# Optimization experiments

Hardware: AMD Instinct MI355X
Metric: run time of the kernel (lower is better)

## Reference

```python
import jax, jax.numpy as jnp
import numpy as np

B, S, E, H, D = 4, 2048, 1024, 16, 64   # batch, seq, embed, heads, head_dim
NUM_BUCKETS, MAX_DISTANCE = 32, 128


def _relative_position_bucket(relative_position, num_buckets, max_distance):
    # causal T5-style bucketing
    max_exact = num_buckets // 2
    max_distance = max(max_distance, max_exact + 1)
    distance = jnp.maximum(-relative_position, 0)
    is_small = distance < max_exact
    safe_distance = jnp.maximum(distance, 1)
    log_scale = jnp.log(safe_distance / max_exact) / jnp.log(max_distance / max_exact)
    large_bucket = max_exact + (log_scale * (num_buckets - max_exact)).astype(jnp.int32)
    large_bucket = jnp.minimum(large_bucket, num_buckets - 1)
    return jnp.where(is_small, distance, large_bucket)


def setup_inputs() -> dict:
    key = jax.random.key(0)
    ks = jax.random.split(key, 7)
    w_scale = 1.0 / np.sqrt(E)
    inputs_q = jax.random.normal(ks[0], (B, S, E), jnp.float32)
    inputs_kv = jax.random.normal(ks[1], (B, S, E), jnp.float32)
    Wq = jax.random.normal(ks[2], (E, H * D), jnp.float32) * w_scale
    Wk = jax.random.normal(ks[3], (E, H * D), jnp.float32) * w_scale
    Wv = jax.random.normal(ks[4], (E, H * D), jnp.float32) * w_scale
    Wo = jax.random.normal(ks[5], (H * D, E), jnp.float32) * (1.0 / np.sqrt(H * D))
    rel_bias = jax.random.normal(ks[6], (H, NUM_BUCKETS), jnp.float32) * 0.02
    mask = jnp.tril(jnp.ones((S, S), dtype=bool))[None, None]  # [1,1,Q,K] causal
    return {"inputs_q": inputs_q, "inputs_kv": inputs_kv, "mask": mask,
            "Wq": Wq, "Wk": Wk, "Wv": Wv, "Wo": Wo, "rel_bias": rel_bias}


def reference(inputs_q, inputs_kv, mask, Wq, Wk, Wv, Wo, rel_bias):
    batch, q_len, embed = inputs_q.shape
    k_len = inputs_kv.shape[1]
    q = (inputs_q @ Wq).reshape(batch, q_len, H, D)
    k = (inputs_kv @ Wk).reshape(batch, k_len, H, D)
    v = (inputs_kv @ Wv).reshape(batch, k_len, H, D)
    attention = jnp.einsum("bqhd,bkhd->bhqk", q, k) * (1.0 / jnp.sqrt(D))
    # T5 relative position bias
    rel_pos = jnp.arange(k_len, dtype=jnp.int32)[None, :] - jnp.arange(q_len, dtype=jnp.int32)[:, None]
    bucket = _relative_position_bucket(rel_pos, NUM_BUCKETS, MAX_DISTANCE)  # [Q,K]
    attention = attention + jnp.take(rel_bias, bucket, axis=1)[None]  # [1,H,Q,K]
    attention = jnp.where(mask, attention, jnp.finfo(jnp.float32).min)
    normalized = jax.nn.softmax(attention, axis=-1)
    output = jnp.einsum("bhqk,bkhd->bqhd", normalized, v).reshape(batch, q_len, H * D)
    return output @ Wo
```

## Files before the change

### kernel.cpp

```cpp
#include <hip/hip_runtime.h>

typedef unsigned short u16;
typedef unsigned int u32;
typedef __bf16 bf16x8 __attribute__((ext_vector_type(8)));
typedef float f32x2 __attribute__((ext_vector_type(2)));
typedef float f32x4 __attribute__((ext_vector_type(4)));
typedef float f32x16 __attribute__((ext_vector_type(16)));

#define S_LEN 2048
#define EMB 1024
#define NH 16
#define HD 64
#define LOG2E 1.44269504088896f
#define QSCALE (0.125f * LOG2E)
#define THRL 11.5415603f
#define FB(r) ((((r) ^ ((r) >> 2))) & 3)

__device__ __forceinline__ u16 f2bf(float f) {
  union { float f; unsigned u; } v; v.f = f;
  unsigned r = (v.u + 0x7fffu + ((v.u >> 16) & 1u)) >> 16;
  return (u16)r;
}

__device__ __forceinline__ u32 packbf(float a, float b) {
  union { __bf16 h[2]; u32 u; } x;
  x.h[0] = (__bf16)a; x.h[1] = (__bf16)b;
  return x.u;
}

__device__ __forceinline__ void g2l16(const void* g, void* l) {
  __builtin_amdgcn_global_load_lds(
      (const unsigned int __attribute__((address_space(1)))*)g,
      (unsigned int __attribute__((address_space(3)))*)l, 16, 0, 0);
}

__device__ __forceinline__ float permswap_max(float a) {
  auto r = __builtin_amdgcn_permlane32_swap(__float_as_int(a), __float_as_int(a), false, false);
  return fmaxf(__int_as_float(r[0]), __int_as_float(r[1]));
}
__device__ __forceinline__ float permswap_add(float a) {
  auto r = __builtin_amdgcn_permlane32_swap(__float_as_int(a), __float_as_int(a), false, false);
  return __int_as_float(r[0]) + __int_as_float(r[1]);
}

__device__ __forceinline__ void phase_end() {
  asm volatile("s_waitcnt lgkmcnt(0)" ::: "memory");
  asm volatile("s_waitcnt vmcnt(0)" ::: "memory");
  __builtin_amdgcn_s_barrier();
  asm volatile("" ::: "memory");
}


__global__ void cvt_bf16_2(const float* __restrict__ aq, const float* __restrict__ akv,
                           u16* __restrict__ dq, u16* __restrict__ dkv) {
  int i = blockIdx.x * blockDim.x + threadIdx.x;
  const float4* s;
  ushort4* d;
  int j;
  if (i < 2097152) {
    s = (const float4*)aq; d = (ushort4*)dq; j = i;
  } else {
    s = (const float4*)akv; d = (ushort4*)dkv; j = i - 2097152;
  }
  float4 f = s[j];
  ushort4 o;
  o.x = f2bf(f.x); o.y = f2bf(f.y); o.z = f2bf(f.z); o.w = f2bf(f.w);
  d[j] = o;
}

__global__ void transcvt4(const float* __restrict__ W0, const float* __restrict__ W1,
                          const float* __restrict__ W2, const float* __restrict__ W3,
                          u16* __restrict__ Dqkv, u16* __restrict__ Do) {
  __shared__ float t[32][33];
  const int z = blockIdx.z;
  const float* W = (z == 0) ? W0 : (z == 1) ? W1 : (z == 2) ? W2 : W3;
  u16* Wt = (z < 3) ? (Dqkv + (size_t)z * 1048576) : Do;
  int k0 = blockIdx.x * 32, n0 = blockIdx.y * 32;
  int tx = threadIdx.x & 31, ty = threadIdx.x >> 5;
#pragma unroll
  for (int i = 0; i < 4; i++) t[ty + i * 8][tx] = W[(k0 + ty + i * 8) * 1024 + n0 + tx];
  __syncthreads();
#pragma unroll
  for (int i = 0; i < 4; i++) Wt[(n0 + ty + i * 8) * 1024 + k0 + tx] = f2bf(t[tx][ty + i * 8]);
}

__global__ void build_bias(const float* __restrict__ rel, float* __restrict__ tbl) {
  int i = blockIdx.x * 256 + threadIdx.x;
  int h = i >> 11, dist = i & 2047;
  int bk;
  if (dist < 16) {
    bk = dist;
  } else {
    float ls = logf((float)dist * (1.0f / 16.0f)) * (1.0f / logf(8.0f));
    bk = 16 + (int)(ls * 16.0f);
    if (bk > 31) bk = 31;
  }
  tbl[i] = rel[h * 32 + bk] * LOG2E;
}


__global__ __launch_bounds__(256, 4) void gemm_qkv(const u16* __restrict__ Aq,
                                                   const u16* __restrict__ Akv,
                                                   const u16* __restrict__ Wt,
                                                   u16* __restrict__ QKV, float qscale) {
  constexpr int K = EMB;
  __shared__ u16 As[2][128 * 32];
  __shared__ u16 Bs[2][128 * 32];

  const int bid = blockIdx.x;
  const int xcd = bid & 7, idx = bid >> 3;
  const int mt = xcd * 8 + (idx & 7);
  const int nt = idx >> 3;
  const int m0 = mt * 128;
  const int n0 = nt * 128;
  const int mat = n0 >> 10;
  const u16* A = (mat == 0) ? Aq : Akv;

  const int tid = threadIdx.x;
  const int lane = tid & 63;
  const int wid = tid >> 6;
  const int wm = (wid >> 1) * 64;
  const int wn = (wid & 1) * 64;
  const int la = lane & 15;
  const int lg = lane >> 4;

  const int r0 = tid >> 2;
  const int c0 = ((tid & 3) ^ FB(r0)) * 8;
  const u16* gA = A + (size_t)(m0 + r0) * K + c0;
  const u16* gB = Wt + (size_t)(n0 + r0) * K + c0;

  f32x4 acc[4][4] = {};

  g2l16(gA, As[0] + tid * 8);
  g2l16(gA + 64 * K, As[0] + tid * 8 + 2048);
  g2l16(gB, Bs[0] + tid * 8);
  g2l16(gB + 64 * K, Bs[0] + tid * 8 + 2048);
  gA += 32;
  gB += 32;
  asm volatile("s_waitcnt vmcnt(0)" ::: "memory");
  __builtin_amdgcn_s_barrier();
  asm volatile("" ::: "memory");

  for (int t = 0; t < 32; ++t) {
    const int cur = t & 1;
    if (t < 31) {
      u16* lA = As[cur ^ 1] + tid * 8;
      u16* lB = Bs[cur ^ 1] + tid * 8;
      g2l16(gA, lA);
      g2l16(gA + 64 * K, lA + 2048);
      g2l16(gB, lB);
      g2l16(gB + 64 * K, lB + 2048);
      gA += 32;
      gB += 32;
    }

    bf16x8 af[4], bb[4];
#pragma unroll
    for (int mf = 0; mf < 4; mf++) {
      int row = wm + mf * 16 + la;
      af[mf] = *(const bf16x8*)&As[cur][row * 32 + ((lg ^ FB(row)) << 3)];
    }
#pragma unroll
    for (int nf = 0; nf < 4; nf++) {
      int row = wn + nf * 16 + la;
      bb[nf] = *(const bf16x8*)&Bs[cur][row * 32 + ((lg ^ FB(row)) << 3)];
    }
    __builtin_amdgcn_s_setprio(1);
#pragma unroll
    for (int mf = 0; mf < 4; mf++)
#pragma unroll
      for (int nf = 0; nf < 4; nf++)
        acc[mf][nf] =
            __builtin_amdgcn_mfma_f32_16x16x32_bf16(af[mf], bb[nf], acc[mf][nf], 0, 0, 0);
    __builtin_amdgcn_s_setprio(0);

    phase_end();
  }

  const float sc = (mat == 0) ? qscale : 1.0f;
#pragma unroll
  for (int mf = 0; mf < 4; mf++)
#pragma unroll
    for (int nf = 0; nf < 4; nf++)
#pragma unroll
      for (int r = 0; r < 4; r++) {
        int m = m0 + wm + mf * 16 + lg * 4 + r;
        int n = n0 + wn + nf * 16 + la;
        float v = acc[mf][nf][r] * sc;
        int b = m >> 11, s = m & 2047, h = (n >> 6) & 15, d = n & 63;
        size_t base = (size_t)mat << 23;
        if (mat < 2)
          QKV[base + (((size_t)(b * 16 + h) * 2048 + s) << 6) + d] = f2bf(v);
        else
          QKV[base + (((size_t)(b * 16 + h) * 64 + d) << 11) + s] = f2bf(v);
      }
}


__global__ __launch_bounds__(256, 4) void gemm_out(const u16* __restrict__ A,
                                                   const u16* __restrict__ Bt,
                                                   float* __restrict__ C) {
  constexpr int K = EMB;
  __shared__ u16 As[2][128 * 32];
  __shared__ u16 Bs[2][128 * 32];
  const int bid = blockIdx.x;
  const int xcd = bid & 7, idx = bid >> 3;
  const int mt = xcd * 8 + (idx & 7);
  const int nt = idx >> 3;
  const int m0 = mt * 128;
  const int n0 = nt * 128;
  const int tid = threadIdx.x;
  const int lane = tid & 63;
  const int wid = tid >> 6;
  const int wm = (wid >> 1) * 64;
  const int wn = (wid & 1) * 64;
  const int la = lane & 15;
  const int lg = lane >> 4;

  const int r0 = tid >> 2;
  const int c0 = ((tid & 3) ^ FB(r0)) * 8;
  const u16* gA = A + (size_t)(m0 + r0) * K + c0;
  const u16* gB = Bt + (size_t)(n0 + r0) * K + c0;

  f32x4 acc[4][4] = {};

  g2l16(gA, As[0] + tid * 8);
  g2l16(gA + 64 * K, As[0] + tid * 8 + 2048);
  g2l16(gB, Bs[0] + tid * 8);
  g2l16(gB + 64 * K, Bs[0] + tid * 8 + 2048);
  gA += 32;
  gB += 32;
  asm volatile("s_waitcnt vmcnt(0)" ::: "memory");
  __builtin_amdgcn_s_barrier();
  asm volatile("" ::: "memory");

  for (int t = 0; t < 32; ++t) {
    const int cur = t & 1;
    if (t < 31) {
      u16* lA = As[cur ^ 1] + tid * 8;
      u16* lB = Bs[cur ^ 1] + tid * 8;
      g2l16(gA, lA);
      g2l16(gA + 64 * K, lA + 2048);
      g2l16(gB, lB);
      g2l16(gB + 64 * K, lB + 2048);
      gA += 32;
      gB += 32;
    }

    bf16x8 af[4], bb[4];
#pragma unroll
    for (int mf = 0; mf < 4; mf++) {
      int row = wm + mf * 16 + la;
      af[mf] = *(const bf16x8*)&As[cur][row * 32 + ((lg ^ FB(row)) << 3)];
    }
#pragma unroll
    for (int nf = 0; nf < 4; nf++) {
      int row = wn + nf * 16 + la;
      bb[nf] = *(const bf16x8*)&Bs[cur][row * 32 + ((lg ^ FB(row)) << 3)];
    }
    __builtin_amdgcn_s_setprio(1);
#pragma unroll
    for (int mf = 0; mf < 4; mf++)
#pragma unroll
      for (int nf = 0; nf < 4; nf++)
        acc[mf][nf] =
            __builtin_amdgcn_mfma_f32_16x16x32_bf16(af[mf], bb[nf], acc[mf][nf], 0, 0, 0);
    __builtin_amdgcn_s_setprio(0);

    phase_end();
  }

#pragma unroll
  for (int mf = 0; mf < 4; mf++)
#pragma unroll
    for (int nf = 0; nf < 4; nf++)
#pragma unroll
      for (int r = 0; r < 4; r++) {
        int m = m0 + wm + mf * 16 + lg * 4 + r;
        int n = n0 + wn + nf * 16 + la;
        C[(size_t)m * 1024 + n] = acc[mf][nf][r];
      }
}


__device__ __forceinline__ void softmax_repack(const f32x16* sacc, int kv0, int qw, int q, int hi,
                                               const float* bias_s, float bias31, float& mrun,
                                               float& lrun, f32x16& o0, f32x16& o1,
                                               u32 (&paw)[4][4]) {
  f32x2 pf[16];
  float adde = 0.f;
  if (kv0 + 176 <= qw) {
#pragma unroll
    for (int j = 0; j < 16; j++) {
      const int nf = j >> 3, r = (j & 7) * 2;
      pf[j] = (f32x2){sacc[nf][r], sacc[nf][r + 1]};
    }
    adde = bias31;
  } else {
    const int qb2 = q - kv0 - 4 * hi;
    const float* bp = bias_s + (qb2 - 59);
    if (kv0 + 63 <= qw) {
#pragma unroll
      for (int j = 0; j < 16; j++) {
        const int nf = j >> 3, r = (j & 7) * 2;
        const int Cn = nf * 32 + (r & 3) + ((r >> 2) << 3);
        f32x2 bv = {bp[59 - Cn], bp[58 - Cn]};
        pf[j] = (f32x2){sacc[nf][r], sacc[nf][r + 1]} + bv;
      }
    } else {
#pragma unroll
      for (int j = 0; j < 16; j++) {
        const int nf = j >> 3, r = (j & 7) * 2;
        const int Cn = nf * 32 + (r & 3) + ((r >> 2) << 3);
        pf[j].x = (Cn <= qb2) ? (sacc[nf][r] + bp[59 - Cn]) : -1e30f;
        pf[j].y = (Cn + 1 <= qb2) ? (sacc[nf][r + 1] + bp[58 - Cn]) : -1e30f;
      }
    }
  }

  f32x2 t8[8];
#pragma unroll
  for (int i = 0; i < 8; i++) t8[i] = __builtin_elementwise_max(pf[i], pf[i + 8]);
#pragma unroll
  for (int i = 0; i < 4; i++) t8[i] = __builtin_elementwise_max(t8[i], t8[i + 4]);
  f32x2 m2 = __builtin_elementwise_max(__builtin_elementwise_max(t8[0], t8[1]),
                                       __builtin_elementwise_max(t8[2], t8[3]));
  float mt = fmaxf(m2.x, m2.y) + adde;
  mt = permswap_max(mt);

  if (__any(mt > mrun + THRL)) {
    float mn = fmaxf(mrun, mt);
    float s = exp2f(mrun - mn);
    mrun = mn;
    lrun *= s;
    o0 *= s;
    o1 *= s;
  }
  const f32x2 ec2 = {adde - mrun, adde - mrun};

  f32x2 s8[8];
#pragma unroll
  for (int j = 0; j < 16; j++) {
    f32x2 a = pf[j] + ec2;
    f32x2 p = {exp2f(a.x), exp2f(a.y)};
    pf[j] = p;
    if (j < 8) s8[j] = p;
    else s8[j - 8] += p;
  }
#pragma unroll
  for (int i = 0; i < 4; i++) s8[i] += s8[i + 4];
  f32x2 s2 = (s8[0] + s8[1]) + (s8[2] + s8[3]);
  lrun += permswap_add(s2.x + s2.y);

#pragma unroll
  for (int ks = 0; ks < 4; ks++) {
    const int j0b = (ks >> 1) * 8 + (ks & 1) * 4;
#pragma unroll
    for (int half = 0; half < 2; half++) {
      u32 Y0 = packbf(pf[j0b + half].x, pf[j0b + half].y);
      u32 Y1 = packbf(pf[j0b + 2 + half].x, pf[j0b + 2 + half].y);
      auto r = __builtin_amdgcn_permlane32_swap((int)Y0, (int)Y1, false, false);
      paw[ks][half] = (u32)r[0];
      paw[ks][2 + half] = (u32)r[1];
    }
  }
}

template <int CUR>
__device__ __forceinline__ void tile_body(int t, int ntblk, int qmax, int qw, int q, int hi,
                                          int la, int tid, const u16*& kp, const u16*& vp,
                                          u16 (*Ks)[64 * 64], u16 (*Vs)[64 * 64],
                                          const bf16x8 (&qfrag)[4], const float* bias_s,
                                          float bias31, float& mrun, float& lrun, f32x16& o0,
                                          f32x16& o1) {
  if (t + 1 < ntblk) {
    u16* lK = Ks[CUR ^ 1] + tid * 8;
    u16* lV = Vs[CUR ^ 1] + tid * 8;
    g2l16(kp, lK);
    g2l16(kp + 32 * 64, lK + 2048);
    g2l16(vp, lV);
    g2l16(vp + 32 * S_LEN, lV + 2048);
    kp += 4096;
    vp += 64;
  }

  const int kv0 = t << 6;
  if (kv0 <= qmax) {
    f32x16 sacc[2] = {};
    __builtin_amdgcn_s_setprio(1);
#pragma unroll
    for (int kk = 0; kk < 4; kk++)
#pragma unroll
      for (int nf = 0; nf < 2; nf++) {
        int row = nf * 32 + la;
        bf16x8 kf = *(const bf16x8*)&Ks[CUR][row * 64 + (((kk * 2 + hi) ^ (row & 7)) << 3)];
        sacc[nf] = __builtin_amdgcn_mfma_f32_32x32x16_bf16(kf, qfrag[kk], sacc[nf], 0, 0, 0);
      }
    __builtin_amdgcn_s_setprio(0);

    u32 paw[4][4];
    softmax_repack(sacc, kv0, qw, q, hi, bias_s, bias31, mrun, lrun, o0, o1, paw);

    __builtin_amdgcn_s_setprio(1);
#pragma unroll
    for (int d2 = 0; d2 < 2; d2++) {
      f32x16& oa = d2 ? o1 : o0;
#pragma unroll
      for (int ks = 0; ks < 4; ks++) {
        int row = d2 * 32 + la;
        bf16x8 vf = *(const bf16x8*)&Vs[CUR][row * 64 + (((ks * 2 + hi) ^ (row & 7)) << 3)];
        union { u32 w[4]; bf16x8 v; } pu;
        pu.w[0] = paw[ks][0]; pu.w[1] = paw[ks][1];
        pu.w[2] = paw[ks][2]; pu.w[3] = paw[ks][3];
        oa = __builtin_amdgcn_mfma_f32_32x32x16_bf16(vf, pu.v, oa, 0, 0, 0);
      }
    }
    __builtin_amdgcn_s_setprio(0);
  }

  phase_end();
}

__global__ __launch_bounds__(256, 3) void attn_kernel(const u16* __restrict__ Qb,
                                                      const u16* __restrict__ Kb,
                                                      const u16* __restrict__ Vtb,
                                                      const float* __restrict__ btbl,
                                                      u16* __restrict__ O) {
  __shared__ u16 Ks[2][64 * 64];
  __shared__ u16 Vs[2][64 * 64];
  __shared__ float bias_s[S_LEN];

  const int bh = blockIdx.x;
  const int h = bh & (NH - 1);
  const int b = bh >> 4;
  const int qt = 15 - blockIdx.y;
  const int q0 = qt * 128;
  const int tid = threadIdx.x;
  const int lane = tid & 63;
  const int w = tid >> 6;
  const int la = lane & 31;
  const int hi = lane >> 5;

  {
    const float4* src = (const float4*)(btbl + h * S_LEN);
    float4* dst = (float4*)bias_s;
    dst[tid] = src[tid];
    dst[tid + 256] = src[tid + 256];
  }

  const u16* Qg = Qb + (size_t)bh * S_LEN * HD;
  const u16* Kg = Kb + (size_t)bh * S_LEN * HD;
  const u16* Vg = Vtb + (size_t)bh * HD * S_LEN;

  const int qw = q0 + w * 32;
  const int q = qw + la;

  bf16x8 qfrag[4];
#pragma unroll
  for (int kk = 0; kk < 4; kk++)
    qfrag[kk] = *(const bf16x8*)&Qg[(size_t)q * HD + kk * 16 + hi * 8];

  f32x16 o0 = {}, o1 = {};
  float mrun = -1e30f;
  float lrun = 0.f;

  const int sr = tid >> 3;
  const int scz = ((tid & 7) ^ (sr & 7)) * 8;
  const u16* kp = Kg + sr * 64 + scz;
  const u16* vp = Vg + (size_t)sr * S_LEN + scz;

  const int ntblk = (q0 + 128) >> 6;
  const int qmax = qw + 31;

  g2l16(kp, Ks[0] + tid * 8);
  g2l16(kp + 32 * 64, Ks[0] + tid * 8 + 2048);
  g2l16(vp, Vs[0] + tid * 8);
  g2l16(vp + 32 * S_LEN, Vs[0] + tid * 8 + 2048);
  kp += 4096;
  vp += 64;
  phase_end();

  const float bias31 = bias_s[S_LEN - 1];

  int t = 0;
  while (t < ntblk) {
    tile_body<0>(t, ntblk, qmax, qw, q, hi, la, tid, kp, vp, Ks, Vs, qfrag, bias_s, bias31,
                 mrun, lrun, o0, o1);
    ++t;
    tile_body<1>(t, ntblk, qmax, qw, q, hi, la, tid, kp, vp, Ks, Vs, qfrag, bias_s, bias31,
                 mrun, lrun, o0, o1);
    ++t;
  }

  const float inv = 1.0f / lrun;
  u16* Og = O + ((size_t)(b * S_LEN + q)) * EMB + h * HD;
#pragma unroll
  for (int d2 = 0; d2 < 2; d2++) {
    const f32x16& oa = d2 ? o1 : o0;
#pragma unroll
    for (int g = 0; g < 4; g++) {
      ushort4 ov;
      ov.x = f2bf(oa[g * 4 + 0] * inv);
      ov.y = f2bf(oa[g * 4 + 1] * inv);
      ov.z = f2bf(oa[g * 4 + 2] * inv);
      ov.w = f2bf(oa[g * 4 + 3] * inv);
      *(ushort4*)&Og[d2 * 32 + g * 8 + hi * 4] = ov;
    }
  }
}


extern "C" void kernel_launch(void* const* d_in, const int* in_sizes, int n_in, void* d_out,
                              int out_size, void* d_ws, size_t ws_size, hipStream_t stream) {
  (void)in_sizes; (void)n_in; (void)out_size; (void)ws_size;
  const float* inq = (const float*)d_in[0];
  const float* inkv = (const float*)d_in[1];
  const float* Wq = (const float*)d_in[3];
  const float* Wk = (const float*)d_in[4];
  const float* Wv = (const float*)d_in[5];
  const float* Wo = (const float*)d_in[6];
  const float* rel = (const float*)d_in[7];
  float* out = (float*)d_out;

  char* ws = (char*)d_ws;
  size_t off = 0;
  auto alloc = [&](size_t bytes) {
    void* p = ws + off;
    off += (bytes + 255) & ~(size_t)255;
    return p;
  };
  u16* Aq = (u16*)alloc(16777216);
  u16* Akv = (u16*)alloc(16777216);
  u16* Wqkvt = (u16*)alloc(6291456);
  u16* Wot = (u16*)alloc(2097152);
  u16* QKV = (u16*)alloc(50331648);
  u16* Ob = (u16*)alloc(16777216);
  float* btbl = (float*)alloc(131072);

  u16* Qb = QKV;
  u16* Kb = QKV + 8388608;
  u16* Vtb = QKV + 16777216;

  cvt_bf16_2<<<16384, 256, 0, stream>>>(inq, inkv, Aq, Akv);
  transcvt4<<<dim3(32, 32, 4), 256, 0, stream>>>(Wq, Wk, Wv, Wo, Wqkvt, Wot);
  build_bias<<<128, 256, 0, stream>>>(rel, btbl);

  gemm_qkv<<<1536, 256, 0, stream>>>(Aq, Akv, Wqkvt, QKV, QSCALE);
  attn_kernel<<<dim3(64, 16), 256, 0, stream>>>(Qb, Kb, Vtb, btbl, Ob);
  gemm_out<<<512, 256, 0, stream>>>(Ob, Wot, out);
}
```

Before: 214.8 us.

## Rewrite QKV GEMM as 256x256 tile with 8 waves and ping-pong pipeline

The QKV projection GEMM moves from 128x128 tiles with 4 waves to 256x256 tiles with 8 waves (512 threads, one block per CU) and a K-step of 64. Each tile is split into 128-row halves in double-buffered LDS. Loads are interleaved with four MFMA sub-phases per stage, using barriers and partial vmcnt waits. The larger tile raises operand reuse and cuts global traffic per FLOP, while the interleaved schedule tries to overlap LDS reads, global loads and MFMA. The cost is 128KB of LDS, many barriers, lower occupancy and fewer blocks (384), which could hurt tail balance.

```diff
diff --git a/kernel.cpp b/kernel.cpp
--- a/kernel.cpp
+++ b/kernel.cpp
@@ -15,6 +15,7 @@
 #define QSCALE (0.125f * LOG2E)
 #define THRL 11.5415603f
 #define FB(r) ((((r) ^ ((r) >> 2))) & 3)
+#define MEMB asm volatile("" ::: "memory")
 
 __device__ __forceinline__ u16 f2bf(float f) {
   union { float f; unsigned u; } v; v.f = f;
@@ -47,7 +48,7 @@
   asm volatile("s_waitcnt lgkmcnt(0)" ::: "memory");
   asm volatile("s_waitcnt vmcnt(0)" ::: "memory");
   __builtin_amdgcn_s_barrier();
-  asm volatile("" ::: "memory");
+  MEMB;
 }
 
 
@@ -99,101 +100,151 @@
 }
 
 
-__global__ __launch_bounds__(256, 4) void gemm_qkv(const u16* __restrict__ Aq,
+__global__ __launch_bounds__(512, 1) void gemm_qkv(const u16* __restrict__ Aq,
                                                    const u16* __restrict__ Akv,
                                                    const u16* __restrict__ Wt,
                                                    u16* __restrict__ QKV, float qscale) {
   constexpr int K = EMB;
-  __shared__ u16 As[2][128 * 32];
-  __shared__ u16 Bs[2][128 * 32];
+  __shared__ u16 Ab[2][2][128 * 64];
+  __shared__ u16 Bb[2][2][128 * 64];
 
   const int bid = blockIdx.x;
   const int xcd = bid & 7, idx = bid >> 3;
-  const int mt = xcd * 8 + (idx & 7);
-  const int nt = idx >> 3;
-  const int m0 = mt * 128;
-  const int n0 = nt * 128;
+  const int mt = xcd * 4 + (idx & 3);
+  const int nt = idx >> 2;
+  const int m0 = mt * 256, n0 = nt * 256;
   const int mat = n0 >> 10;
   const u16* A = (mat == 0) ? Aq : Akv;
 
   const int tid = threadIdx.x;
-  const int lane = tid & 63;
-  const int wid = tid >> 6;
-  const int wm = (wid >> 1) * 64;
-  const int wn = (wid & 1) * 64;
-  const int la = lane & 15;
-  const int lg = lane >> 4;
-
-  const int r0 = tid >> 2;
-  const int c0 = ((tid & 3) ^ FB(r0)) * 8;
-  const u16* gA = A + (size_t)(m0 + r0) * K + c0;
-  const u16* gB = Wt + (size_t)(n0 + r0) * K + c0;
-
-  f32x4 acc[4][4] = {};
-
-  g2l16(gA, As[0] + tid * 8);
-  g2l16(gA + 64 * K, As[0] + tid * 8 + 2048);
-  g2l16(gB, Bs[0] + tid * 8);
-  g2l16(gB + 64 * K, Bs[0] + tid * 8 + 2048);
-  gA += 32;
-  gB += 32;
-  asm volatile("s_waitcnt vmcnt(0)" ::: "memory");
+  const int lane = tid & 63, w = tid >> 6;
+  const int wsm = w >> 2, wsn = w & 3;
+  const int la = lane & 15, lg = lane >> 4;
+
+  const int srow = tid >> 3;
+  const int gcol = ((tid & 7) ^ (srow & 7)) * 8;
+  const u16* Abase = A + (size_t)(m0 + srow) * K + gcol;
+  const u16* Bbase = Wt + (size_t)(n0 + srow) * K + gcol;
+
+  auto stA = [&](int db, int h, int kt) {
+    const u16* s = Abase + (size_t)(h * 128) * K + kt * 64;
+    u16* d = &Ab[db][h][tid * 8];
+    g2l16(s, d);
+    g2l16(s + (size_t)64 * K, d + 4096);
+  };
+  auto stB = [&](int db, int h, int kt) {
+    const u16* s = Bbase + (size_t)(h * 128) * K + kt * 64;
+    u16* d = &Bb[db][h][tid * 8];
+    g2l16(s, d);
+    g2l16(s + (size_t)64 * K, d + 4096);
+  };
+
+  f32x4 acc[2][2][4][2] = {};
+  bf16x8 afr[4][2], bfr[2][2];
+
+  auto rdA = [&](int db, int h) {
+#pragma unroll
+    for (int mf = 0; mf < 4; mf++) {
+      const int row = wsm * 64 + mf * 16 + la;
+#pragma unroll
+      for (int ks = 0; ks < 2; ks++)
+        afr[mf][ks] =
+            *(const bf16x8*)&Ab[db][h][row * 64 + ((((ks << 2) + lg) ^ (row & 7)) << 3)];
+    }
+  };
+  auto rdB = [&](int db, int h) {
+#pragma unroll
+    for (int nf = 0; nf < 2; nf++) {
+      const int row = wsn * 32 + nf * 16 + la;
+#pragma unroll
+      for (int ks = 0; ks < 2; ks++)
+        bfr[nf][ks] =
+            *(const bf16x8*)&Bb[db][h][row * 64 + ((((ks << 2) + lg) ^ (row & 7)) << 3)];
+    }
+  };
+  auto mfma = [&](int mh, int nh) {
+    __builtin_amdgcn_s_setprio(1);
+#pragma unroll
+    for (int mf = 0; mf < 4; mf++)
+#pragma unroll
+      for (int nf = 0; nf < 2; nf++)
+#pragma unroll
+        for (int ks = 0; ks < 2; ks++)
+          acc[mh][nh][mf][nf] = __builtin_amdgcn_mfma_f32_16x16x32_bf16(
+              afr[mf][ks], bfr[nf][ks], acc[mh][nh][mf][nf], 0, 0, 0);
+    __builtin_amdgcn_s_setprio(0);
+  };
+  auto bar_pre = [&] {
+    MEMB;
+    __builtin_amdgcn_s_barrier();
+    asm volatile("s_waitcnt lgkmcnt(0)" ::: "memory");
+  };
+  auto bar_post = [&] {
+    MEMB;
+    __builtin_amdgcn_s_barrier();
+    MEMB;
+  };
+
+  stA(0, 0, 0); stB(0, 0, 0); stB(0, 1, 0); stA(0, 1, 0);
+  stA(1, 0, 1); stB(1, 0, 1);
+  asm volatile("s_waitcnt vmcnt(4)" ::: "memory");
   __builtin_amdgcn_s_barrier();
-  asm volatile("" ::: "memory");
-
-  for (int t = 0; t < 32; ++t) {
-    const int cur = t & 1;
-    if (t < 31) {
-      u16* lA = As[cur ^ 1] + tid * 8;
-      u16* lB = Bs[cur ^ 1] + tid * 8;
-      g2l16(gA, lA);
-      g2l16(gA + 64 * K, lA + 2048);
-      g2l16(gB, lB);
-      g2l16(gB + 64 * K, lB + 2048);
-      gA += 32;
-      gB += 32;
-    }
-
-    bf16x8 af[4], bb[4];
-#pragma unroll
-    for (int mf = 0; mf < 4; mf++) {
-      int row = wm + mf * 16 + la;
-      af[mf] = *(const bf16x8*)&As[cur][row * 32 + ((lg ^ FB(row)) << 3)];
-    }
-#pragma unroll
-    for (int nf = 0; nf < 4; nf++) {
-      int row = wn + nf * 16 + la;
-      bb[nf] = *(const bf16x8*)&Bs[cur][row * 32 + ((lg ^ FB(row)) << 3)];
-    }
-    __builtin_amdgcn_s_setprio(1);
-#pragma unroll
-    for (int mf = 0; mf < 4; mf++)
-#pragma unroll
-      for (int nf = 0; nf < 4; nf++)
-        acc[mf][nf] =
-            __builtin_amdgcn_mfma_f32_16x16x32_bf16(af[mf], bb[nf], acc[mf][nf], 0, 0, 0);
-    __builtin_amdgcn_s_setprio(0);
-
-    phase_end();
+  MEMB;
+
+#pragma unroll 1
+  for (int i = 0; i < 8; ++i) {
+    const int o = 2 * i + 1, e2 = 2 * i + 2, o2 = 2 * i + 3;
+    const bool more = (i < 7);
+    rdA(0, 0); rdB(0, 0);
+    stA(1, 1, o); stB(1, 1, o);
+    bar_pre(); mfma(0, 0); bar_post();
+    rdB(0, 1);
+    bar_pre(); mfma(0, 1); bar_post();
+    rdA(0, 1); rdB(0, 0);
+    if (more) stA(0, 0, e2);
+    bar_pre(); mfma(1, 0); bar_post();
+    rdB(0, 1);
+    if (more) stB(0, 0, e2);
+    bar_pre(); mfma(1, 1);
+    if (more) asm volatile("s_waitcnt vmcnt(4)" ::: "memory");
+    else      asm volatile("s_waitcnt vmcnt(0)" ::: "memory");
+    bar_post();
+    rdA(1, 0); rdB(1, 0);
+    if (more) { stA(0, 1, e2); stB(0, 1, e2); }
+    bar_pre(); mfma(0, 0); bar_post();
+    rdB(1, 1);
+    bar_pre(); mfma(0, 1); bar_post();
+    rdA(1, 1); rdB(1, 0);
+    if (more) stA(1, 0, o2);
+    bar_pre(); mfma(1, 0); bar_post();
+    rdB(1, 1);
+    if (more) stB(1, 0, o2);
+    bar_pre(); mfma(1, 1);
+    if (more) asm volatile("s_waitcnt vmcnt(4)" ::: "memory");
+    bar_post();
   }
 
   const float sc = (mat == 0) ? qscale : 1.0f;
-#pragma unroll
-  for (int mf = 0; mf < 4; mf++)
-#pragma unroll
-    for (int nf = 0; nf < 4; nf++)
-#pragma unroll
-      for (int r = 0; r < 4; r++) {
-        int m = m0 + wm + mf * 16 + lg * 4 + r;
-        int n = n0 + wn + nf * 16 + la;
-        float v = acc[mf][nf][r] * sc;
-        int b = m >> 11, s = m & 2047, h = (n >> 6) & 15, d = n & 63;
-        size_t base = (size_t)mat << 23;
-        if (mat < 2)
-          QKV[base + (((size_t)(b * 16 + h) * 2048 + s) << 6) + d] = f2bf(v);
-        else
-          QKV[base + (((size_t)(b * 16 + h) * 64 + d) << 11) + s] = f2bf(v);
-      }
+  const size_t base = (size_t)mat << 23;
+#pragma unroll
+  for (int mh = 0; mh < 2; mh++)
+#pragma unroll
+    for (int nh = 0; nh < 2; nh++)
+#pragma unroll
+      for (int mf = 0; mf < 4; mf++)
+#pragma unroll
+        for (int nf = 0; nf < 2; nf++)
+#pragma unroll
+          for (int r = 0; r < 4; r++) {
+            int m = m0 + mh * 128 + wsm * 64 + mf * 16 + lg * 4 + r;
+            int n = n0 + nh * 128 + wsn * 32 + nf * 16 + la;
+            float v = acc[mh][nh][mf][nf][r] * sc;
+            int b = m >> 11, s = m & 2047, hh = (n >> 6) & 15, d = n & 63;
+            if (mat < 2)
+              QKV[base + (((size_t)(b * 16 + hh) * 2048 + s) << 6) + d] = f2bf(v);
+            else
+              QKV[base + (((size_t)(b * 16 + hh) * 64 + d) << 11) + s] = f2bf(v);
+          }
 }
 
 
@@ -232,7 +283,7 @@
   gB += 32;
   asm volatile("s_waitcnt vmcnt(0)" ::: "memory");
   __builtin_amdgcn_s_barrier();
-  asm volatile("" ::: "memory");
+  MEMB;
 
   for (int t = 0; t < 32; ++t) {
     const int cur = t & 1;
@@ -545,7 +596,7 @@
   transcvt4<<<dim3(32, 32, 4), 256, 0, stream>>>(Wq, Wk, Wv, Wo, Wqkvt, Wot);
   build_bias<<<128, 256, 0, stream>>>(rel, btbl);
 
-  gemm_qkv<<<1536, 256, 0, stream>>>(Aq, Akv, Wqkvt, QKV, QSCALE);
+  gemm_qkv<<<384, 512, 0, stream>>>(Aq, Akv, Wqkvt, QKV, QSCALE);
   attn_kernel<<<dim3(64, 16), 256, 0, stream>>>(Qb, Kb, Vtb, btbl, Ob);
   gemm_out<<<512, 256, 0, stream>>>(Ob, Wot, out);
 }
```

After: 221.9 us. +3.3%, slower.
